# Kernel tuning notes

Hardware: AMD Instinct MI355X
Metric: run time of the kernel (lower is better)

## Reference

```python
import jax, jax.numpy as jnp
import numpy as np

TEMPERATURE = 0.07
B, D = 8192, 1024
EPS = 1e-08


def setup_inputs() -> dict:
    key = jax.random.key(0)
    k1, k2, k3, k4, k5 = jax.random.split(key, 5)
    visual_feats = jax.random.normal(k1, (B, D), dtype=jnp.float32)
    textual_feats = jax.random.normal(k2, (B, D), dtype=jnp.float32)
    transport_matrix = jax.random.uniform(k3, (B, B), dtype=jnp.float32)
    confident_clean_mask = jax.random.randint(k4, (B,), 0, 2).astype(jnp.bool_)
    confident_noisy_mask = jax.random.randint(k5, (B,), 0, 2).astype(jnp.bool_)
    return {
        'visual_feats': visual_feats,
        'textual_feats': textual_feats,
        'transport_matrix': transport_matrix,
        'confident_clean_mask': confident_clean_mask,
        'confident_noisy_mask': confident_noisy_mask,
    }


def _l2norm(x):
    # matches F.normalize(p=2, dim=-1) with default eps=1e-12
    n = jnp.sqrt(jnp.sum(x * x, axis=-1, keepdims=True))
    return x / jnp.maximum(n, 1e-12)


def reference(visual_feats, textual_feats, transport_matrix,
              confident_clean_mask, confident_noisy_mask):
    # current_epoch defaults to 0 < push_phase_epochs -> 'push_only' phase:
    # progressive_loss = CCL complementary (negative-push) loss.
    n = confident_noisy_mask.astype(jnp.float32)  # [B]
    # negative_mask[i,j] = 1 if (i==j and noisy[i]) or (i!=j and (noisy[i] or noisy[j]))
    # at i==j, max(n[i],n[i]) == n[i], so the broadcast max covers both cases.
    negative_mask = jnp.maximum(n[:, None], n[None, :])  # [B, B]

    v = _l2norm(visual_feats)
    t = _l2norm(textual_feats)
    similarities = v @ t.T  # [B, B]

    logits = similarities / TEMPERATURE
    neg_sum = jnp.sum(jnp.exp(logits) * negative_mask, axis=1) + EPS  # [B]
    progressive_loss = jnp.mean(jnp.log(neg_sum))
    return progressive_loss
```

## Files before the change

### kernel.cpp

```cpp
#include <hip/hip_runtime.h>
#include <hip/hip_bf16.h>

#define NB 8192
#define ND 1024

typedef __attribute__((ext_vector_type(8))) short bf16x8;
typedef __attribute__((ext_vector_type(4))) float f32x4;

__device__ __forceinline__ void async16(const void* g, void* l) {
  __builtin_amdgcn_global_load_lds(
      (const __attribute__((address_space(1))) void*)g,
      (__attribute__((address_space(3))) void*)l,
      16, 0, 0);
}

__device__ __forceinline__ unsigned short f2bf(float f) {
  union { float f; unsigned u; } a; a.f = f;
  unsigned u = a.u;
  return (unsigned short)((u + 0x7fffu + ((u >> 16) & 1u)) >> 16);
}

__global__ void prep_mask(const unsigned char* __restrict__ raw,
                          float* __restrict__ nmask) {
  __shared__ int flag;
  if (threadIdx.x == 0) flag = 0;
  __syncthreads();
  int any = 0;
  for (int i = threadIdx.x; i < NB; i += 256)
    if ((i & 3) != 0 && raw[i] != 0) any = 1;
  if (any) atomicOr(&flag, 1);
  __syncthreads();
  if (flag) {
    for (int i = threadIdx.x; i < NB; i += 256)
      nmask[i] = raw[i] ? 1.0f : 0.0f;
  } else {
    const int* ri = (const int*)raw;
    for (int i = threadIdx.x; i < NB; i += 256)
      nmask[i] = ri[i] ? 1.0f : 0.0f;
  }
}

__global__ void norm_cast(const float* __restrict__ vis,
                          const float* __restrict__ txt,
                          unsigned short* __restrict__ vb,
                          unsigned short* __restrict__ tb) {
  const float* src = blockIdx.y ? txt : vis;
  unsigned short* dst = blockIdx.y ? tb : vb;
  int row = blockIdx.x;
  int t = threadIdx.x;
  float4 x = ((const float4*)(src + (size_t)row * ND))[t];
  float ss = x.x * x.x + x.y * x.y + x.z * x.z + x.w * x.w;
  #pragma unroll
  for (int m = 32; m; m >>= 1) ss += __shfl_xor(ss, m);
  __shared__ float sred[4];
  if ((t & 63) == 0) sred[t >> 6] = ss;
  __syncthreads();
  float tot = sred[0] + sred[1] + sred[2] + sred[3];
  float inv = 1.0f / fmaxf(sqrtf(tot), 1e-12f);
  ushort4 o;
  o.x = f2bf(x.x * inv); o.y = f2bf(x.y * inv);
  o.z = f2bf(x.z * inv); o.w = f2bf(x.w * inv);
  ((ushort4*)dst)[(size_t)row * (ND / 4) + t] = o;
}

__global__ __launch_bounds__(256) void gemm_fused(
    const unsigned short* __restrict__ vb, const unsigned short* __restrict__ tb,
    const float* __restrict__ nmask, float* __restrict__ partial) {
  __shared__ unsigned short As[128 * 64];
  __shared__ unsigned short Bs[128 * 64];
  __shared__ float part2[128][2];

  const int bx = blockIdx.x, by = blockIdx.y;
  const int i0 = by * 128, j0 = bx * 128;
  const int t = threadIdx.x;
  const int w = t >> 6;
  const int l = t & 63;
  const int quad = l >> 4;
  const int l15 = l & 15;
  const int wm = w >> 1, wn = w & 1;
  const int rw = wm * 64, cw = wn * 64;

  const int lrow = l >> 3;
  const int lchunk = (l & 7) ^ lrow;
  const unsigned short* Ag = vb + (size_t)(i0 + w * 32 + lrow) * ND + lchunk * 8;
  const unsigned short* Bg = tb + (size_t)(j0 + w * 32 + lrow) * ND + lchunk * 8;
  char* AsB = (char*)As + w * 32 * 128;
  char* BsB = (char*)Bs + w * 32 * 128;

  f32x4 acc[4][4] = {};

  for (int kb = 0; kb < ND; kb += 64) {
    #pragma unroll
    for (int q = 0; q < 4; ++q) {
      async16(Ag + kb + q * 8 * ND, AsB + q * 1024);
      async16(Bg + kb + q * 8 * ND, BsB + q * 1024);
    }
    __syncthreads();
    #pragma unroll
    for (int kt = 0; kt < 2; ++kt) {
      bf16x8 a[4], b[4];
      #pragma unroll
      for (int mi = 0; mi < 4; ++mi) {
        int r = rw + mi * 16 + l15;
        int pos = (kt * 4 + quad) ^ (r & 7);
        a[mi] = *(const bf16x8*)&As[r * 64 + pos * 8];
      }
      #pragma unroll
      for (int ni = 0; ni < 4; ++ni) {
        int r = cw + ni * 16 + l15;
        int pos = (kt * 4 + quad) ^ (r & 7);
        b[ni] = *(const bf16x8*)&Bs[r * 64 + pos * 8];
      }
      #pragma unroll
      for (int mi = 0; mi < 4; ++mi)
        #pragma unroll
        for (int ni = 0; ni < 4; ++ni)
          acc[mi][ni] = __builtin_amdgcn_mfma_f32_16x16x32_bf16(
              a[mi], b[ni], acc[mi][ni], 0, 0, 0);
    }
    __syncthreads();
  }

  const float SCALE = 20.60992915555662f;
  float ncol[4];
  #pragma unroll
  for (int ni = 0; ni < 4; ++ni) ncol[ni] = nmask[j0 + cw + ni * 16 + l15];

  #pragma unroll
  for (int mi = 0; mi < 4; ++mi) {
    float nrow[4], rowacc[4] = {0.f, 0.f, 0.f, 0.f};
    #pragma unroll
    for (int r = 0; r < 4; ++r) nrow[r] = nmask[i0 + rw + mi * 16 + quad * 4 + r];
    #pragma unroll
    for (int ni = 0; ni < 4; ++ni) {
      #pragma unroll
      for (int r = 0; r < 4; ++r)
        rowacc[r] += exp2f(acc[mi][ni][r] * SCALE) * fmaxf(nrow[r], ncol[ni]);
    }
    #pragma unroll
    for (int r = 0; r < 4; ++r) {
      float v = rowacc[r];
      v += __shfl_xor(v, 1); v += __shfl_xor(v, 2);
      v += __shfl_xor(v, 4); v += __shfl_xor(v, 8);
      if (l15 == 0) part2[rw + mi * 16 + quad * 4 + r][wn] = v;
    }
  }
  __syncthreads();
  if (t < 128)
    partial[(size_t)bx * NB + i0 + t] = part2[t][0] + part2[t][1];
}

__global__ void finalize(const float* __restrict__ partial, float* __restrict__ out) {
  int r = blockIdx.x * 256 + threadIdx.x;
  float s = 0.f;
  #pragma unroll 4
  for (int c = 0; c < 64; ++c) s += partial[(size_t)c * NB + r];
  float lg = logf(s + 1e-8f);
  #pragma unroll
  for (int m = 32; m; m >>= 1) lg += __shfl_xor(lg, m);
  __shared__ float sred[4];
  if ((threadIdx.x & 63) == 0) sred[threadIdx.x >> 6] = lg;
  __syncthreads();
  if (threadIdx.x == 0)
    atomicAdd(out, (sred[0] + sred[1] + sred[2] + sred[3]) * (1.0f / NB));
}

extern "C" void kernel_launch(void* const* d_in, const int* in_sizes, int n_in,
                              void* d_out, int out_size, void* d_ws, size_t ws_size,
                              hipStream_t stream) {
  const float* vis = (const float*)d_in[0];
  const float* txt = (const float*)d_in[1];
  const unsigned char* noisy = (const unsigned char*)d_in[4];
  float* out = (float*)d_out;

  char* ws = (char*)d_ws;
  unsigned short* vb = (unsigned short*)ws;
  unsigned short* tb = (unsigned short*)(ws + ((size_t)16 << 20));
  float* nmask = (float*)(ws + ((size_t)32 << 20));
  float* partial = (float*)(ws + ((size_t)32 << 20) + (64 << 10));

  hipMemsetAsync(d_out, 0, sizeof(float), stream);
  prep_mask<<<1, 256, 0, stream>>>(noisy, nmask);
  norm_cast<<<dim3(NB, 2), 256, 0, stream>>>(vis, txt, vb, tb);
  gemm_fused<<<dim3(NB / 128, NB / 128), 256, 0, stream>>>(vb, tb, nmask, partial);
  finalize<<<NB / 256, 256, 0, stream>>>(partial, out);
}
```

Before: 532.4 us.

## Rewrite fused GEMM with 256x256 tiles, double-buffered LDS and interleaved MFMA schedule

The GEMM kernel moves from 128x128 tiles with 4 waves to 256x256 tiles with 8 waves and double-buffered LDS. Global-to-LDS async loads are interleaved with MFMA quarter-blocks under explicit barriers, vmcnt waits and s_setprio, and the block index is remapped for L2 locality. The goal is to hide load latency and raise arithmetic intensity instead of stalling on a single buffer each K step. In exchange it uses much more LDS (about 128KB per block) and higher register pressure, and it relies on a hand-tuned barrier schedule that is fragile.

```diff
diff --git a/kernel.cpp b/kernel.cpp
--- a/kernel.cpp
+++ b/kernel.cpp
@@ -63,98 +63,156 @@
   ((ushort4*)dst)[(size_t)row * (ND / 4) + t] = o;
 }
 
-__global__ __launch_bounds__(256) void gemm_fused(
+#define AS_BARRIER asm volatile("s_barrier" ::: "memory")
+#define LGKM0 asm volatile("s_waitcnt lgkmcnt(0)" ::: "memory")
+#define VMCNT(n) asm volatile("s_waitcnt vmcnt(" #n ")" ::: "memory")
+
+#define STG(GB, LB, KT, H) do {                                               \
+    async16(GB + (size_t)((H) * 128 + 0) * ND + (KT) * 64,                    \
+            LB + ((H) * 128 + 0) * 128);                                      \
+    async16(GB + (size_t)((H) * 128 + 64) * ND + (KT) * 64,                   \
+            LB + ((H) * 128 + 64) * 128);                                     \
+  } while (0)
+
+#define RDA(BUF, MH, DST) do {                                                \
+    _Pragma("unroll") for (int mi_ = 0; mi_ < 4; ++mi_) {                     \
+      DST[mi_][0] = *(const bf16x8*)&As[BUF][(rA + (MH)*64 + mi_*16)*64 + c0*8]; \
+      DST[mi_][1] = *(const bf16x8*)&As[BUF][(rA + (MH)*64 + mi_*16)*64 + c1*8]; \
+    } } while (0)
+
+#define RDB(BUF) do {                                                         \
+    _Pragma("unroll") for (int ni_ = 0; ni_ < 4; ++ni_) {                     \
+      b[ni_][0] = *(const bf16x8*)&Bs[BUF][(rB + ni_*16)*64 + c0*8];          \
+      b[ni_][1] = *(const bf16x8*)&Bs[BUF][(rB + ni_*16)*64 + c1*8];          \
+    } } while (0)
+
+#define MFMAQ(AF, RB, NH) do {                                                \
+    _Pragma("unroll") for (int mi_ = 0; mi_ < 4; ++mi_)                       \
+    _Pragma("unroll") for (int ni_ = 0; ni_ < 2; ++ni_)                       \
+    _Pragma("unroll") for (int kk_ = 0; kk_ < 2; ++kk_)                       \
+      acc[(RB) + mi_][(NH)*2 + ni_] =                                         \
+          __builtin_amdgcn_mfma_f32_16x16x32_bf16(                            \
+              AF[mi_][kk_], b[(NH)*2 + ni_][kk_],                             \
+              acc[(RB) + mi_][(NH)*2 + ni_], 0, 0, 0);                        \
+  } while (0)
+
+__global__ __launch_bounds__(512, 2) void gemm_fused(
     const unsigned short* __restrict__ vb, const unsigned short* __restrict__ tb,
     const float* __restrict__ nmask, float* __restrict__ partial) {
-  __shared__ unsigned short As[128 * 64];
-  __shared__ unsigned short Bs[128 * 64];
-  __shared__ float part2[128][2];
-
-  const int bx = blockIdx.x, by = blockIdx.y;
-  const int i0 = by * 128, j0 = bx * 128;
+  __shared__ unsigned short As[2][256 * 64];
+  __shared__ unsigned short Bs[2][256 * 64];
+  __shared__ float part[256][4];
+
+  int lin = blockIdx.y * 32 + blockIdx.x;
+  lin = (lin & 7) * 128 + (lin >> 3);
+  const int bx = lin & 31, by = lin >> 5;
+  const int i0 = by * 256, j0 = bx * 256;
+
   const int t = threadIdx.x;
-  const int w = t >> 6;
-  const int l = t & 63;
-  const int quad = l >> 4;
-  const int l15 = l & 15;
-  const int wm = w >> 1, wn = w & 1;
-  const int rw = wm * 64, cw = wn * 64;
+  const int w = t >> 6, l = t & 63;
+  const int quad = l >> 4, l15 = l & 15;
+  const int wm = w >> 2, wn = w & 3;
 
   const int lrow = l >> 3;
-  const int lchunk = (l & 7) ^ lrow;
-  const unsigned short* Ag = vb + (size_t)(i0 + w * 32 + lrow) * ND + lchunk * 8;
-  const unsigned short* Bg = tb + (size_t)(j0 + w * 32 + lrow) * ND + lchunk * 8;
-  char* AsB = (char*)As + w * 32 * 128;
-  char* BsB = (char*)Bs + w * 32 * 128;
-
-  f32x4 acc[4][4] = {};
-
-  for (int kb = 0; kb < ND; kb += 64) {
-    #pragma unroll
-    for (int q = 0; q < 4; ++q) {
-      async16(Ag + kb + q * 8 * ND, AsB + q * 1024);
-      async16(Bg + kb + q * 8 * ND, BsB + q * 1024);
-    }
-    __syncthreads();
-    #pragma unroll
-    for (int kt = 0; kt < 2; ++kt) {
-      bf16x8 a[4], b[4];
-      #pragma unroll
-      for (int mi = 0; mi < 4; ++mi) {
-        int r = rw + mi * 16 + l15;
-        int pos = (kt * 4 + quad) ^ (r & 7);
-        a[mi] = *(const bf16x8*)&As[r * 64 + pos * 8];
-      }
-      #pragma unroll
-      for (int ni = 0; ni < 4; ++ni) {
-        int r = cw + ni * 16 + l15;
-        int pos = (kt * 4 + quad) ^ (r & 7);
-        b[ni] = *(const bf16x8*)&Bs[r * 64 + pos * 8];
-      }
-      #pragma unroll
-      for (int mi = 0; mi < 4; ++mi)
-        #pragma unroll
-        for (int ni = 0; ni < 4; ++ni)
-          acc[mi][ni] = __builtin_amdgcn_mfma_f32_16x16x32_bf16(
-              a[mi], b[ni], acc[mi][ni], 0, 0, 0);
-    }
-    __syncthreads();
+  const int lch = (l & 7) ^ lrow;
+  const unsigned short* Ag = vb + (size_t)(i0 + w * 8 + lrow) * ND + lch * 8;
+  const unsigned short* Bg = tb + (size_t)(j0 + w * 8 + lrow) * ND + lch * 8;
+  char* AL0 = (char*)&As[0][0] + w * 1024;
+  char* AL1 = (char*)&As[1][0] + w * 1024;
+  char* BL0 = (char*)&Bs[0][0] + w * 1024;
+  char* BL1 = (char*)&Bs[1][0] + w * 1024;
+
+  const int rA = wm * 128 + l15;
+  const int rB = wn * 64 + l15;
+  const int c0 = quad ^ (l & 7);
+  const int c1 = (4 + quad) ^ (l & 7);
+
+  STG(Ag, AL0, 0, 0); STG(Ag, AL0, 0, 1);
+  STG(Bg, BL0, 0, 0); STG(Bg, BL0, 0, 1);
+  STG(Ag, AL1, 1, 0); STG(Ag, AL1, 1, 1);
+  VMCNT(4);
+  AS_BARRIER;
+
+  bf16x8 a[4][2], a2[4][2], b[4][2];
+  f32x4 acc[8][4] = {};
+
+  #pragma unroll 1
+  for (int tt = 0; tt < 8; ++tt) {
+    const int k0 = 2 * tt, k1 = 2 * tt + 1;
+    const bool pf = (tt < 7);
+    RDB(0); RDA(0, 0, a);
+    STG(Bg, BL1, k1, 0);
+    AS_BARRIER; LGKM0;
+    __builtin_amdgcn_s_setprio(1); MFMAQ(a, 0, 0); __builtin_amdgcn_s_setprio(0);
+    AS_BARRIER;
+    RDA(0, 1, a2);
+    STG(Bg, BL1, k1, 1);
+    AS_BARRIER; LGKM0;
+    __builtin_amdgcn_s_setprio(1); MFMAQ(a, 0, 1); __builtin_amdgcn_s_setprio(0);
+    AS_BARRIER;
+    if (pf) STG(Ag, AL0, k0 + 2, 0);
+    AS_BARRIER;
+    __builtin_amdgcn_s_setprio(1); MFMAQ(a2, 4, 0); __builtin_amdgcn_s_setprio(0);
+    AS_BARRIER;
+    if (pf) { STG(Ag, AL0, k0 + 2, 1); VMCNT(4); } else { VMCNT(0); }
+    AS_BARRIER;
+    __builtin_amdgcn_s_setprio(1); MFMAQ(a2, 4, 1); __builtin_amdgcn_s_setprio(0);
+    AS_BARRIER;
+    RDB(1); RDA(1, 0, a);
+    if (pf) STG(Bg, BL0, k0 + 2, 0);
+    AS_BARRIER; LGKM0;
+    __builtin_amdgcn_s_setprio(1); MFMAQ(a, 0, 0); __builtin_amdgcn_s_setprio(0);
+    AS_BARRIER;
+    RDA(1, 1, a2);
+    if (pf) STG(Bg, BL0, k0 + 2, 1);
+    AS_BARRIER; LGKM0;
+    __builtin_amdgcn_s_setprio(1); MFMAQ(a, 0, 1); __builtin_amdgcn_s_setprio(0);
+    AS_BARRIER;
+    if (pf) STG(Ag, AL1, k1 + 2, 0);
+    AS_BARRIER;
+    __builtin_amdgcn_s_setprio(1); MFMAQ(a2, 4, 0); __builtin_amdgcn_s_setprio(0);
+    AS_BARRIER;
+    if (pf) { STG(Ag, AL1, k1 + 2, 1); VMCNT(4); }
+    AS_BARRIER;
+    __builtin_amdgcn_s_setprio(1); MFMAQ(a2, 4, 1); __builtin_amdgcn_s_setprio(0);
+    AS_BARRIER;
   }
 
   const float SCALE = 20.60992915555662f;
   float ncol[4];
   #pragma unroll
-  for (int ni = 0; ni < 4; ++ni) ncol[ni] = nmask[j0 + cw + ni * 16 + l15];
-
-  #pragma unroll
-  for (int mi = 0; mi < 4; ++mi) {
-    float nrow[4], rowacc[4] = {0.f, 0.f, 0.f, 0.f};
+  for (int ni = 0; ni < 4; ++ni) ncol[ni] = nmask[j0 + wn * 64 + ni * 16 + l15];
+
+  #pragma unroll
+  for (int mi = 0; mi < 8; ++mi) {
+    float nrow[4], ra[4] = {0.f, 0.f, 0.f, 0.f};
     #pragma unroll
-    for (int r = 0; r < 4; ++r) nrow[r] = nmask[i0 + rw + mi * 16 + quad * 4 + r];
+    for (int r = 0; r < 4; ++r)
+      nrow[r] = nmask[i0 + wm * 128 + mi * 16 + quad * 4 + r];
     #pragma unroll
-    for (int ni = 0; ni < 4; ++ni) {
+    for (int ni = 0; ni < 4; ++ni)
       #pragma unroll
       for (int r = 0; r < 4; ++r)
-        rowacc[r] += exp2f(acc[mi][ni][r] * SCALE) * fmaxf(nrow[r], ncol[ni]);
-    }
+        ra[r] += exp2f(acc[mi][ni][r] * SCALE) * fmaxf(nrow[r], ncol[ni]);
     #pragma unroll
     for (int r = 0; r < 4; ++r) {
-      float v = rowacc[r];
+      float v = ra[r];
       v += __shfl_xor(v, 1); v += __shfl_xor(v, 2);
       v += __shfl_xor(v, 4); v += __shfl_xor(v, 8);
-      if (l15 == 0) part2[rw + mi * 16 + quad * 4 + r][wn] = v;
+      if (l15 == 0) part[wm * 128 + mi * 16 + quad * 4 + r][wn] = v;
     }
   }
   __syncthreads();
-  if (t < 128)
-    partial[(size_t)bx * NB + i0 + t] = part2[t][0] + part2[t][1];
+  if (t < 256)
+    partial[(size_t)bx * NB + i0 + t] =
+        part[t][0] + part[t][1] + part[t][2] + part[t][3];
 }
 
 __global__ void finalize(const float* __restrict__ partial, float* __restrict__ out) {
   int r = blockIdx.x * 256 + threadIdx.x;
   float s = 0.f;
   #pragma unroll 4
-  for (int c = 0; c < 64; ++c) s += partial[(size_t)c * NB + r];
+  for (int c = 0; c < 32; ++c) s += partial[(size_t)c * NB + r];
   float lg = logf(s + 1e-8f);
   #pragma unroll
   for (int m = 32; m; m >>= 1) lg += __shfl_xor(lg, m);
@@ -182,6 +240,6 @@
   hipMemsetAsync(d_out, 0, sizeof(float), stream);
   prep_mask<<<1, 256, 0, stream>>>(noisy, nmask);
   norm_cast<<<dim3(NB, 2), 256, 0, stream>>>(vis, txt, vb, tb);
-  gemm_fused<<<dim3(NB / 128, NB / 128), 256, 0, stream>>>(vb, tb, nmask, partial);
+  gemm_fused<<<dim3(NB / 256, NB / 256), 512, 0, stream>>>(vb, tb, nmask, partial);
   finalize<<<NB / 256, 256, 0, stream>>>(partial, out);
 }
```

Measured after the change: 506.3 us. -4.9%, faster.
